# Optimization experiments

Hardware: AMD Instinct MI355X
Metric: run time of the kernel (lower is better)

The kernel has to match this reference:

```python
import jax, jax.numpy as jnp
import numpy as np

N_HEADS = 16
MAX_REL = 64  # max_relative_pos_len


def setup_inputs() -> dict:
    key = jax.random.key(0)
    ks = jax.random.split(key, 8)
    B, S, D = 2, 2048, 1024
    d = D // N_HEADS
    sc = 0.02
    return {
        "hidden_states": jax.random.normal(ks[0], (B, S, D), jnp.float32),
        "attention_mask": jnp.zeros((B, 1, 1, S), jnp.float32),
        "Wq": jax.random.normal(ks[1], (D, D), jnp.float32) * sc,
        "bq": jnp.zeros((D,), jnp.float32),
        "Wk": jax.random.normal(ks[2], (D, D), jnp.float32) * sc,
        "bk": jnp.zeros((D,), jnp.float32),
        "Wv": jax.random.normal(ks[3], (D, D), jnp.float32) * sc,
        "bv": jnp.zeros((D,), jnp.float32),
        "emb_k": jax.random.normal(ks[4], (2 * MAX_REL + 1, d), jnp.float32) * sc,
        "emb_v": jax.random.normal(ks[5], (2 * MAX_REL + 1, d), jnp.float32) * sc,
    }


def reference(hidden_states, attention_mask, Wq, bq, Wk, bk, Wv, bv, emb_k, emb_v):
    B, S, D = hidden_states.shape
    H = N_HEADS
    d = D // H
    scale = 1.0 / jnp.sqrt(jnp.asarray(d, hidden_states.dtype))

    def heads(x):  # [B,S,D] -> [B,H,S,d]
        return x.reshape(B, S, H, d).transpose(0, 2, 1, 3)

    q = heads(hidden_states @ Wq + bq)
    k = heads(hidden_states @ Wk + bk)
    v = heads(hidden_states @ Wv + bv)

    # relative position indices, clamped: [S_q, S_k]
    rel_idx = jnp.clip(jnp.arange(S)[:, None] - jnp.arange(S)[None, :], -MAX_REL, MAX_REL) + MAX_REL
    rel_k = emb_k[rel_idx]  # [S, S, d]

    # content scores + relative-key bias, both scaled by 1/sqrt(d)
    scores = (jnp.einsum('bhqd,bhkd->bhqk', q, k)
              + jnp.einsum('bhqd,qkd->bhqk', q, rel_k)) * scale
    scores = scores + attention_mask
    probs = jax.nn.softmax(scores, axis=-1)  # dropout is identity at p=0

    rel_v = emb_v[rel_idx]  # [S, S, d]
    ctx = (jnp.einsum('bhqk,bhkd->bhqd', probs, v)
           + jnp.einsum('bhqk,qkd->bhqd', probs, rel_v))
    return ctx.transpose(0, 2, 1, 3).reshape(B, S, D)
```

## Files before the change

### kernel.cpp

```cpp
#include <hip/hip_runtime.h>
#include <stdint.h>

typedef unsigned short u16;
typedef __attribute__((ext_vector_type(8))) short short8;
typedef __attribute__((ext_vector_type(4))) short s16x4;
typedef __attribute__((ext_vector_type(4))) float f32x4;
typedef __attribute__((ext_vector_type(4))) unsigned short u16x4;

#define S_LEN 2048
#define NH 16
#define DMODEL 1024
#define NR 129
#define LOG2E 1.44269504f

#define MFMA(a,b,c) __builtin_amdgcn_mfma_f32_16x16x32_bf16((a),(b),(c),0,0,0)

__device__ __forceinline__ u16 f2bf(float f){
  uint32_t u = __float_as_uint(f);
  u += 0x7fff + ((u >> 16) & 1);
  return (u16)(u >> 16);
}
__device__ __forceinline__ u16 f2bfa(float f){
  return (u16)((__float_as_uint(f) + 0x8000u) >> 16);
}
__device__ __forceinline__ float bf2f(u16 h){ return __uint_as_float(((uint32_t)h) << 16); }

__global__ __launch_bounds__(256) void k_prep(const float* __restrict__ X,
                                              const float* __restrict__ Wq, const float* __restrict__ Wk,
                                              const float* __restrict__ Wv, const float* __restrict__ Wemb,
                                              const float* __restrict__ mask,
                                              u16* __restrict__ Xb, u16* __restrict__ Wt,
                                              u16* __restrict__ Eb, float* __restrict__ maskL){
  const int bid = blockIdx.x, tid = threadIdx.x;
  if (bid < 4096){
    int i = bid * 256 + tid;
    const float4* xp = (const float4*)X;
    float4 v = xp[i];
    u16x4 o; o.x = f2bf(v.x); o.y = f2bf(v.y); o.z = f2bf(v.z); o.w = f2bf(v.w);
    *(u16x4*)(Xb + (size_t)i * 4) = o;
  } else if (bid < 4864){
    int b2 = bid - 4096;
    int z = b2 >> 8;
    const float* W = (z == 0) ? Wq : (z == 1) ? Wk : Wv;
    u16* Ot = Wt + (size_t)z * 1024 * 1024;
    __shared__ float t[64][65];
    int k0 = ((b2 >> 4) & 15) * 64, n0 = (b2 & 15) * 64;
    int c = tid & 63, r0 = (tid >> 6) * 16;
    #pragma unroll
    for (int i = 0; i < 16; ++i) t[r0 + i][c] = W[(size_t)(k0 + r0 + i) * 1024 + n0 + c];
    __syncthreads();
    #pragma unroll
    for (int i = 0; i < 16; ++i) Ot[(size_t)(n0 + r0 + i) * 1024 + k0 + c] = f2bf(t[c][r0 + i]);
  } else if (bid < 4900){
    int idx = (bid - 4864) * 256 + tid;
    if (idx < 144 * 64){
      int r = idx >> 6;
      Eb[idx] = (r < NR) ? f2bf(Wemb[idx]) : (u16)0;
    }
  } else {
    int idx = (bid - 4900) * 256 + tid;
    maskL[idx] = mask[idx] * LOG2E;
  }
}

__global__ __launch_bounds__(256) void k_qkv(const u16* __restrict__ Xb, const u16* __restrict__ Wt,
                                             const float* __restrict__ bq, const float* __restrict__ bk,
                                             const float* __restrict__ bv,
                                             u16* __restrict__ Qs, u16* __restrict__ Kb, u16* __restrict__ Vb){
  const int z = blockIdx.z;
  const u16* W = Wt + (size_t)z * 1024 * 1024;
  const float* bias = (z == 0) ? bq : (z == 1) ? bk : bv;
  u16* outp = (z == 0) ? Qs : (z == 1) ? Kb : Vb;
  const float vs = (z == 0) ? 0.125f * LOG2E : 1.0f;
  const int n0 = blockIdx.x * 128, m0 = blockIdx.y * 128;
  const int tid = threadIdx.x, w = tid >> 6, lane = tid & 63, l15 = lane & 15, quad = lane >> 4;
  const int wm = (w >> 1) * 64, wn = (w & 1) * 64;
  __shared__ __attribute__((aligned(16))) u16 As[128][40];
  __shared__ __attribute__((aligned(16))) u16 Bs[128][40];
  f32x4 acc[4][4];
  #pragma unroll
  for (int i = 0; i < 4; ++i)
    #pragma unroll
    for (int j = 0; j < 4; ++j) acc[i][j] = (f32x4){0.f,0.f,0.f,0.f};

  for (int k0 = 0; k0 < 1024; k0 += 32){
    __syncthreads();
    #pragma unroll
    for (int i = 0; i < 2; ++i){
      int c = tid + i * 256; int r = c >> 2, ch = (c & 3) * 8;
      *(short8*)&As[r][ch] = *(const short8*)(Xb + (size_t)(m0 + r) * 1024 + k0 + ch);
      *(short8*)&Bs[r][ch] = *(const short8*)(W  + (size_t)(n0 + r) * 1024 + k0 + ch);
    }
    __syncthreads();
    short8 af[4], bfr[4];
    #pragma unroll
    for (int f = 0; f < 4; ++f){
      af[f]  = *(const short8*)&As[wm + f * 16 + l15][quad * 8];
      bfr[f] = *(const short8*)&Bs[wn + f * 16 + l15][quad * 8];
    }
    #pragma unroll
    for (int i = 0; i < 4; ++i)
      #pragma unroll
      for (int j = 0; j < 4; ++j) acc[i][j] = MFMA(af[i], bfr[j], acc[i][j]);
  }
  #pragma unroll
  for (int i = 0; i < 4; ++i){
    #pragma unroll
    for (int j = 0; j < 4; ++j){
      int col = n0 + wn + j * 16 + l15;
      float bsv = bias[col];
      int hh = col >> 6, jd = col & 63;
      #pragma unroll
      for (int r = 0; r < 4; ++r){
        int row = m0 + wm + i * 16 + quad * 4 + r;
        int bb = row >> 11, s = row & 2047;
        float vv = (acc[i][j][r] + bsv) * vs;
        outp[(((size_t)(bb * 16 + hh)) * S_LEN + s) * 64 + jd] = f2bf(vv);
      }
    }
  }
}

__global__ __launch_bounds__(256) void k_transv(const u16* __restrict__ Vb, u16* __restrict__ Vt){
  const int g = blockIdx.y; const int s0 = blockIdx.x * 64;
  __shared__ __attribute__((aligned(16))) u16 t[64][72];
  const int tid = threadIdx.x;
  #pragma unroll
  for (int i = 0; i < 2; ++i){
    int c = tid + i * 256; int r = c >> 3, ch = (c & 7) * 8;
    *(short8*)&t[r][ch] = *(const short8*)(Vb + ((size_t)g * S_LEN + s0 + r) * 64 + ch);
  }
  __syncthreads();
  #pragma unroll
  for (int i = 0; i < 2; ++i){
    int c = tid + i * 256; int d = c >> 3, ch = (c & 7) * 8;
    short8 vv;
    #pragma unroll
    for (int u = 0; u < 8; ++u) vv[u] = (short)t[ch + u][d];
    *(short8*)(Vt + ((size_t)g * 64 + d) * S_LEN + s0 + ch) = vv;
  }
}

__global__ __launch_bounds__(256, 3) void k_flash(const u16* __restrict__ QS, const u16* __restrict__ KB,
                                                  const u16* __restrict__ VT, const u16* __restrict__ EMBK,
                                                  const float* __restrict__ maskL, const float* __restrict__ embv,
                                                  float* __restrict__ out){
  const int g = blockIdx.y; const int b = g >> 4; const int h = g & 15;
  const int q0 = blockIdx.x * 64;
  const int tid = threadIdx.x;
  const int w = tid >> 6; const int lane = tid & 63;
  const int l15 = lane & 15; const int quad = lane >> 4;
  const int wm = w * 16;
  const int rqb = quad * 4;
  const int qrow = q0 + wm + l15;

  __shared__ union UKE {
    struct {
      __attribute__((aligned(16))) u16 Ks[64][72];
      __attribute__((aligned(16))) u16 Vs[64][72];
    } s;
    __attribute__((aligned(16))) u16 Evs[64][136];
  } uu;
  __shared__ __attribute__((aligned(16))) u16 QEb[4][16][132];
  __shared__ __attribute__((aligned(16))) u16 Psb[64][136];

  {
    short8 z8 = (short8){0,0,0,0,0,0,0,0};
    for (int i = tid; i < 64 * 136 / 8; i += 256) ((short8*)Psb)[i] = z8;
  }

  const u16* qptr = QS + ((size_t)g * S_LEN + q0 + wm + l15) * 64 + quad * 8;
  short8 qa0 = *(const short8*)qptr;
  short8 qa1 = *(const short8*)(qptr + 32);

  #pragma unroll
  for (int fn = 0; fn < 9; ++fn){
    const u16* ep = EMBK + (fn * 16 + l15) * 64 + quad * 8;
    short8 eb0 = *(const short8*)ep;
    short8 eb1 = *(const short8*)(ep + 32);
    f32x4 c = (f32x4){0.f,0.f,0.f,0.f};
    c = MFMA(qa0, eb0, c);
    c = MFMA(qa1, eb1, c);
    int col = fn * 16 + l15;
    if (col < NR){
      #pragma unroll
      for (int r = 0; r < 4; ++r) QEb[w][rqb + r][col] = f2bf(c[r]);
    }
  }
  __syncthreads();

  const float qeR = bf2f(QEb[w][l15][0]);
  const float qeL = bf2f(QEb[w][l15][128]);

  f32x4 o[4];
  #pragma unroll
  for (int f = 0; f < 4; ++f) o[f] = (f32x4){0.f,0.f,0.f,0.f};
  float l_sum = 0.f;
  float ll0   = 0.f;
  float ll_mx = 0.f;
  float rsb_s = 0.f;

  for (int kt = 0; kt < S_LEN; kt += 64){
    __syncthreads();
    #pragma unroll
    for (int i = 0; i < 2; ++i){
      int c = tid + i * 256; int row = c >> 3, ch = (c & 7) * 8;
      *(short8*)&uu.s.Ks[row][ch] = *(const short8*)(KB + ((size_t)g * S_LEN + kt + row) * 64 + ch);
      short8 vsrc = *(const short8*)(VT + ((size_t)g * 64 + row) * S_LEN + kt + ch);
      int c0 = ((ch & 8) ? 32 : 0) + (ch >> 4) * 4;
      s16x4 lo = __builtin_shufflevector(vsrc, vsrc, 0, 1, 2, 3);
      s16x4 hi = __builtin_shufflevector(vsrc, vsrc, 4, 5, 6, 7);
      *(s16x4*)&uu.s.Vs[row][c0]      = lo;
      *(s16x4*)&uu.s.Vs[row][c0 + 16] = hi;
    }
    __syncthreads();

    f32x4 sc[4];
    #pragma unroll
    for (int fn = 0; fn < 4; ++fn){
      short8 kb0 = *(const short8*)&uu.s.Ks[fn * 16 + l15][quad * 8];
      short8 kb1 = *(const short8*)&uu.s.Ks[fn * 16 + l15][32 + quad * 8];
      f32x4 c = (f32x4){0.f,0.f,0.f,0.f};
      c = MFMA(kb0, qa0, c);
      c = MFMA(kb1, qa1, c);
      sc[fn] = c;
    }

    if (kt <= q0 - 128){
      #pragma unroll
      for (int fn = 0; fn < 4; ++fn){
        f32x4 mv = *(const f32x4*)&maskL[b * S_LEN + kt + fn * 16 + rqb];
        mv += qeL;
        #pragma unroll
        for (int r = 0; r < 4; ++r){
          float p = exp2f(sc[fn][r] + mv[r]);
          l_sum += p;
          sc[fn][r] = p;
        }
      }
    } else if (kt >= q0 + 128){
      #pragma unroll
      for (int fn = 0; fn < 4; ++fn){
        f32x4 mv = *(const f32x4*)&maskL[b * S_LEN + kt + fn * 16 + rqb];
        mv += qeR;
        #pragma unroll
        for (int r = 0; r < 4; ++r){
          float p = exp2f(sc[fn][r] + mv[r]);
          l_sum += p;
          sc[fn][r] = p;
        }
      }
    } else {
      #pragma unroll
      for (int fn = 0; fn < 4; ++fn){
        f32x4 mv = *(const f32x4*)&maskL[b * S_LEN + kt + fn * 16 + rqb];
        int kbase = kt + fn * 16 + rqb;
        #pragma unroll
        for (int r = 0; r < 4; ++r){
          int dq = qrow - (kbase + r) + 64;
          int ridx = min(max(dq, 0), 128);
          float p = exp2f(sc[fn][r] + bf2f(QEb[w][l15][ridx]) + mv[r]);
          l_sum += p;
          ll_mx += (dq >= 128) ? p : 0.f;
          if (dq >= 1 && dq <= 127){
            Psb[wm + l15][127 - dq] = f2bfa(p);
            rsb_s += p;
          }
          sc[fn][r] = p;
        }
      }
    }

    #pragma unroll
    for (int fp = 0; fp < 2; ++fp){
      short8 pa;
      #pragma unroll
      for (int r = 0; r < 4; ++r){
        pa[r]     = (short)f2bfa(sc[2 * fp][r]);
        pa[4 + r] = (short)f2bfa(sc[2 * fp + 1][r]);
      }
      #pragma unroll
      for (int fd = 0; fd < 4; ++fd){
        short8 vb = *(const short8*)&uu.s.Vs[fd * 16 + l15][quad * 16 + fp * 8];
        o[fd] = MFMA(pa, vb, o[fd]);
      }
    }

    if (kt == q0 - 128) ll0 = l_sum;
  }

  __syncthreads();
  {
    int d = tid & 63, t4 = tid >> 6;
    #pragma unroll
    for (int it = 0; it < 34; ++it){
      int t = t4 + it * 4;
      float v = (t <= 126) ? embv[(size_t)(127 - t) * 64 + d] : 0.f;
      uu.Evs[d][t] = f2bf(v);
    }
  }
  __syncthreads();

  f32x4 ob[4];
  #pragma unroll
  for (int f = 0; f < 4; ++f) ob[f] = (f32x4){0.f,0.f,0.f,0.f};
  #pragma unroll
  for (int kb = 0; kb < 4; ++kb){
    short8 pa = *(const short8*)&Psb[wm + l15][kb * 32 + quad * 8];
    #pragma unroll
    for (int fd = 0; fd < 4; ++fd){
      short8 vb = *(const short8*)&uu.Evs[fd * 16 + l15][kb * 32 + quad * 8];
      ob[fd] = MFMA(pa, vb, ob[fd]);
    }
  }

  float llv = ll0 + ll_mx;
  #pragma unroll
  for (int st = 16; st < 64; st <<= 1){
    l_sum += __shfl_xor(l_sum, st, 64);
    llv   += __shfl_xor(llv,   st, 64);
    rsb_s += __shfl_xor(rsb_s, st, 64);
  }

  float inv[4], tl[4], trr[4];
  #pragma unroll
  for (int r = 0; r < 4; ++r){
    int src = (quad << 4) + rqb + r;
    float L  = __shfl(l_sum, src, 64);
    float lv = __shfl(llv,   src, 64);
    float rv = __shfl(rsb_s, src, 64);
    inv[r] = 1.f / L;
    tl[r]  = lv * inv[r];
    trr[r] = 1.f - tl[r] - rv * inv[r];
  }

  #pragma unroll
  for (int fd = 0; fd < 4; ++fd){
    int dim = fd * 16 + l15;
    float evL = embv[(size_t)128 * 64 + dim];
    float evR = embv[dim];
    #pragma unroll
    for (int r = 0; r < 4; ++r){
      int row = q0 + wm + rqb + r;
      float val = (o[fd][r] + ob[fd][r]) * inv[r] + tl[r] * evL + trr[r] * evR;
      out[((size_t)(b * S_LEN + row)) * DMODEL + h * 64 + dim] = val;
    }
  }
}

extern "C" void kernel_launch(void* const* d_in, const int* in_sizes, int n_in,
                              void* d_out, int out_size, void* d_ws, size_t ws_size,
                              hipStream_t stream){
  const float* X    = (const float*)d_in[0];
  const float* mask = (const float*)d_in[1];
  const float* Wq   = (const float*)d_in[2];
  const float* bq   = (const float*)d_in[3];
  const float* Wk   = (const float*)d_in[4];
  const float* bk   = (const float*)d_in[5];
  const float* Wv   = (const float*)d_in[6];
  const float* bv   = (const float*)d_in[7];
  const float* embk = (const float*)d_in[8];
  const float* embv = (const float*)d_in[9];
  float* out = (float*)d_out;
  char* ws = (char*)d_ws;

  u16* XB   = (u16*)(ws + 0);
  u16* WT   = (u16*)(ws + 8388608);
  u16* EKB  = (u16*)(ws + 14680064);
  u16* QS   = (u16*)(ws + 14698496);
  u16* KB   = (u16*)(ws + 23087104);
  u16* VB   = (u16*)(ws + 31475712);
  u16* VT   = (u16*)(ws + 39864320);
  float* MSL = (float*)(ws + 48252928);

  k_prep   <<<4916, 256, 0, stream>>>(X, Wq, Wk, Wv, embk, mask, XB, WT, EKB, MSL);
  k_qkv    <<<dim3(8, 32, 3), 256, 0, stream>>>(XB, WT, bq, bk, bv, QS, KB, VB);
  k_transv <<<dim3(32, 32), 256, 0, stream>>>(VB, VT);
  k_flash  <<<dim3(32, 32), 256, 0, stream>>>(QS, KB, VT, EKB, MSL, embv, out);
}
```

Measured before the change: 263.9 us.

## Prefetch K/V tiles into registers, fold mask into MFMA, compute row sums via MFMA

The QKV GEMM now stages tiles with global_load_lds direct-to-LDS copies in an unpadded layout. The attention loop register-prefetches the next K/V tile and mask values while the current tile is processed. It seeds the QK MFMA accumulator with mask plus the relative bias and uses the hardware exp2. Row sums of P come from an extra MFMA against a ones vector instead of scalar adds, and bf16 packing uses v_cvt_pk_bf16_f32, with s_setprio around the MFMA sections. This adds register pressure, and the unpadded LDS layout may cause bank conflicts. Row sums are now taken from bf16-rounded probabilities.

Measured after the change: 213.8 us. -19.0%, faster.

```diff
diff --git a/kernel.cpp b/kernel.cpp
--- a/kernel.cpp
+++ b/kernel.cpp
@@ -24,6 +24,17 @@
   return (u16)((__float_as_uint(f) + 0x8000u) >> 16);
 }
 __device__ __forceinline__ float bf2f(u16 h){ return __uint_as_float(((uint32_t)h) << 16); }
+
+__device__ __forceinline__ uint32_t cvtpk(float lo, float hi){
+  uint32_t r;
+  asm("v_cvt_pk_bf16_f32 %0, %1, %2" : "=v"(r) : "v"(lo), "v"(hi));
+  return r;
+}
+
+__device__ __forceinline__ void gl_lds16(const u16* g, u16* l){
+  __builtin_amdgcn_global_load_lds((const __attribute__((address_space(1))) void*)g,
+                                   (__attribute__((address_space(3))) void*)l, 16, 0, 0);
+}
 
 __global__ __launch_bounds__(256) void k_prep(const float* __restrict__ X,
                                               const float* __restrict__ Wq, const float* __restrict__ Wk,
@@ -75,28 +86,32 @@
   const int n0 = blockIdx.x * 128, m0 = blockIdx.y * 128;
   const int tid = threadIdx.x, w = tid >> 6, lane = tid & 63, l15 = lane & 15, quad = lane >> 4;
   const int wm = (w >> 1) * 64, wn = (w & 1) * 64;
-  __shared__ __attribute__((aligned(16))) u16 As[128][40];
-  __shared__ __attribute__((aligned(16))) u16 Bs[128][40];
+  __shared__ __attribute__((aligned(16))) u16 As[128 * 32];
+  __shared__ __attribute__((aligned(16))) u16 Bs[128 * 32];
   f32x4 acc[4][4];
   #pragma unroll
   for (int i = 0; i < 4; ++i)
     #pragma unroll
     for (int j = 0; j < 4; ++j) acc[i][j] = (f32x4){0.f,0.f,0.f,0.f};
+
+  const int rA = lane >> 2, cA = (lane & 3) * 8;
+  const u16* aBase = Xb + (size_t)(m0 + w * 16 + rA) * 1024 + cA;
+  const u16* bBase = W  + (size_t)(n0 + w * 16 + rA) * 1024 + cA;
+  u16* aDst0 = As + (w * 16) * 32;  u16* aDst1 = As + (64 + w * 16) * 32;
+  u16* bDst0 = Bs + (w * 16) * 32;  u16* bDst1 = Bs + (64 + w * 16) * 32;
 
   for (int k0 = 0; k0 < 1024; k0 += 32){
     __syncthreads();
-    #pragma unroll
-    for (int i = 0; i < 2; ++i){
-      int c = tid + i * 256; int r = c >> 2, ch = (c & 3) * 8;
-      *(short8*)&As[r][ch] = *(const short8*)(Xb + (size_t)(m0 + r) * 1024 + k0 + ch);
-      *(short8*)&Bs[r][ch] = *(const short8*)(W  + (size_t)(n0 + r) * 1024 + k0 + ch);
-    }
+    gl_lds16(aBase + k0,             aDst0);
+    gl_lds16(aBase + 64 * 1024 + k0, aDst1);
+    gl_lds16(bBase + k0,             bDst0);
+    gl_lds16(bBase + 64 * 1024 + k0, bDst1);
     __syncthreads();
     short8 af[4], bfr[4];
     #pragma unroll
     for (int f = 0; f < 4; ++f){
-      af[f]  = *(const short8*)&As[wm + f * 16 + l15][quad * 8];
-      bfr[f] = *(const short8*)&Bs[wn + f * 16 + l15][quad * 8];
+      af[f]  = *(const short8*)(As + (wm + f * 16 + l15) * 32 + quad * 8);
+      bfr[f] = *(const short8*)(Bs + (wn + f * 16 + l15) * 32 + quad * 8);
     }
     #pragma unroll
     for (int i = 0; i < 4; ++i)
@@ -169,6 +184,22 @@
     for (int i = tid; i < 64 * 136 / 8; i += 256) ((short8*)Psb)[i] = z8;
   }
 
+  const int srow0 = tid >> 3;
+  const int srow1 = srow0 + 32;
+  const int sch = (tid & 7) * 8;
+  const int c0 = ((sch & 8) ? 32 : 0) + (sch >> 4) * 4;
+  const u16* kSrc = KB + (size_t)g * S_LEN * 64 + sch;
+  const u16* vSrc = VT + (size_t)g * 64 * S_LEN + sch;
+  const float* mBase = maskL + b * S_LEN;
+
+  short8 kr0 = *(const short8*)(kSrc + (size_t)srow0 * 64);
+  short8 kr1 = *(const short8*)(kSrc + (size_t)srow1 * 64);
+  short8 vr0 = *(const short8*)(vSrc + (size_t)srow0 * S_LEN);
+  short8 vr1 = *(const short8*)(vSrc + (size_t)srow1 * S_LEN);
+  f32x4 mcur[4];
+  #pragma unroll
+  for (int fn = 0; fn < 4; ++fn) mcur[fn] = *(const f32x4*)(mBase + fn * 16 + rqb);
+
   const u16* qptr = QS + ((size_t)g * S_LEN + q0 + wm + l15) * 64 + quad * 8;
   short8 qa0 = *(const short8*)qptr;
   short8 qa1 = *(const short8*)(qptr + 32);
@@ -192,101 +223,117 @@
   const float qeR = bf2f(QEb[w][l15][0]);
   const float qeL = bf2f(QEb[w][l15][128]);
 
+  short8 bones;
+  {
+    short one = (l15 == 0) ? (short)0x3F80 : (short)0;
+    #pragma unroll
+    for (int j = 0; j < 8; ++j) bones[j] = one;
+  }
+
   f32x4 o[4];
   #pragma unroll
   for (int f = 0; f < 4; ++f) o[f] = (f32x4){0.f,0.f,0.f,0.f};
-  float l_sum = 0.f;
-  float ll0   = 0.f;
+  f32x4 lacc = (f32x4){0.f,0.f,0.f,0.f};
+  float ll0v[4] = {0.f,0.f,0.f,0.f};
   float ll_mx = 0.f;
   float rsb_s = 0.f;
 
   for (int kt = 0; kt < S_LEN; kt += 64){
     __syncthreads();
-    #pragma unroll
-    for (int i = 0; i < 2; ++i){
-      int c = tid + i * 256; int row = c >> 3, ch = (c & 7) * 8;
-      *(short8*)&uu.s.Ks[row][ch] = *(const short8*)(KB + ((size_t)g * S_LEN + kt + row) * 64 + ch);
-      short8 vsrc = *(const short8*)(VT + ((size_t)g * 64 + row) * S_LEN + kt + ch);
-      int c0 = ((ch & 8) ? 32 : 0) + (ch >> 4) * 4;
-      s16x4 lo = __builtin_shufflevector(vsrc, vsrc, 0, 1, 2, 3);
-      s16x4 hi = __builtin_shufflevector(vsrc, vsrc, 4, 5, 6, 7);
-      *(s16x4*)&uu.s.Vs[row][c0]      = lo;
-      *(s16x4*)&uu.s.Vs[row][c0 + 16] = hi;
+    *(short8*)&uu.s.Ks[srow0][sch] = kr0;
+    *(short8*)&uu.s.Ks[srow1][sch] = kr1;
+    {
+      s16x4 lo = __builtin_shufflevector(vr0, vr0, 0, 1, 2, 3);
+      s16x4 hi = __builtin_shufflevector(vr0, vr0, 4, 5, 6, 7);
+      *(s16x4*)&uu.s.Vs[srow0][c0]      = lo;
+      *(s16x4*)&uu.s.Vs[srow0][c0 + 16] = hi;
+    }
+    {
+      s16x4 lo = __builtin_shufflevector(vr1, vr1, 0, 1, 2, 3);
+      s16x4 hi = __builtin_shufflevector(vr1, vr1, 4, 5, 6, 7);
+      *(s16x4*)&uu.s.Vs[srow1][c0]      = lo;
+      *(s16x4*)&uu.s.Vs[srow1][c0 + 16] = hi;
     }
     __syncthreads();
 
-    f32x4 sc[4];
+    const int ktn = kt + 64;
+    f32x4 mnext[4];
+    if (ktn < S_LEN){
+      kr0 = *(const short8*)(kSrc + (size_t)(ktn + srow0) * 64);
+      kr1 = *(const short8*)(kSrc + (size_t)(ktn + srow1) * 64);
+      vr0 = *(const short8*)(vSrc + (size_t)srow0 * S_LEN + ktn);
+      vr1 = *(const short8*)(vSrc + (size_t)srow1 * S_LEN + ktn);
+      #pragma unroll
+      for (int fn = 0; fn < 4; ++fn) mnext[fn] = *(const f32x4*)(mBase + ktn + fn * 16 + rqb);
+    }
+
+    const bool leftC  = (kt <= q0 - 128);
+    const bool rightC = (kt >= q0 + 128);
+    const float qeadd = leftC ? qeL : (rightC ? qeR : 0.f);
+
+    f32x4 p4[4];
+    __builtin_amdgcn_s_setprio(1);
     #pragma unroll
     for (int fn = 0; fn < 4; ++fn){
       short8 kb0 = *(const short8*)&uu.s.Ks[fn * 16 + l15][quad * 8];
       short8 kb1 = *(const short8*)&uu.s.Ks[fn * 16 + l15][32 + quad * 8];
-      f32x4 c = (f32x4){0.f,0.f,0.f,0.f};
+      f32x4 c = mcur[fn] + qeadd;
       c = MFMA(kb0, qa0, c);
       c = MFMA(kb1, qa1, c);
-      sc[fn] = c;
-    }
-
-    if (kt <= q0 - 128){
+      p4[fn] = c;
+    }
+    __builtin_amdgcn_s_setprio(0);
+
+    if (leftC | rightC){
+      #pragma unroll
+      for (int fn = 0; fn < 4; ++fn)
+        #pragma unroll
+        for (int r = 0; r < 4; ++r) p4[fn][r] = __builtin_amdgcn_exp2f(p4[fn][r]);
+    } else {
       #pragma unroll
       for (int fn = 0; fn < 4; ++fn){
-        f32x4 mv = *(const f32x4*)&maskL[b * S_LEN + kt + fn * 16 + rqb];
-        mv += qeL;
-        #pragma unroll
-        for (int r = 0; r < 4; ++r){
-          float p = exp2f(sc[fn][r] + mv[r]);
-          l_sum += p;
-          sc[fn][r] = p;
-        }
-      }
-    } else if (kt >= q0 + 128){
-      #pragma unroll
-      for (int fn = 0; fn < 4; ++fn){
-        f32x4 mv = *(const f32x4*)&maskL[b * S_LEN + kt + fn * 16 + rqb];
-        mv += qeR;
-        #pragma unroll
-        for (int r = 0; r < 4; ++r){
-          float p = exp2f(sc[fn][r] + mv[r]);
-          l_sum += p;
-          sc[fn][r] = p;
-        }
-      }
-    } else {
-      #pragma unroll
-      for (int fn = 0; fn < 4; ++fn){
-        f32x4 mv = *(const f32x4*)&maskL[b * S_LEN + kt + fn * 16 + rqb];
         int kbase = kt + fn * 16 + rqb;
         #pragma unroll
         for (int r = 0; r < 4; ++r){
           int dq = qrow - (kbase + r) + 64;
           int ridx = min(max(dq, 0), 128);
-          float p = exp2f(sc[fn][r] + bf2f(QEb[w][l15][ridx]) + mv[r]);
-          l_sum += p;
+          float p = __builtin_amdgcn_exp2f(p4[fn][r] + bf2f(QEb[w][l15][ridx]));
           ll_mx += (dq >= 128) ? p : 0.f;
           if (dq >= 1 && dq <= 127){
             Psb[wm + l15][127 - dq] = f2bfa(p);
             rsb_s += p;
           }
-          sc[fn][r] = p;
+          p4[fn][r] = p;
         }
       }
     }
 
+    __builtin_amdgcn_s_setprio(1);
     #pragma unroll
     for (int fp = 0; fp < 2; ++fp){
-      short8 pa;
-      #pragma unroll
-      for (int r = 0; r < 4; ++r){
-        pa[r]     = (short)f2bfa(sc[2 * fp][r]);
-        pa[4 + r] = (short)f2bfa(sc[2 * fp + 1][r]);
-      }
+      union { uint32_t u[4]; short8 s8; } pk;
+      pk.u[0] = cvtpk(p4[2 * fp][0],     p4[2 * fp][1]);
+      pk.u[1] = cvtpk(p4[2 * fp][2],     p4[2 * fp][3]);
+      pk.u[2] = cvtpk(p4[2 * fp + 1][0], p4[2 * fp + 1][1]);
+      pk.u[3] = cvtpk(p4[2 * fp + 1][2], p4[2 * fp + 1][3]);
+      short8 pa = pk.s8;
+      lacc = MFMA(pa, bones, lacc);
       #pragma unroll
       for (int fd = 0; fd < 4; ++fd){
         short8 vb = *(const short8*)&uu.s.Vs[fd * 16 + l15][quad * 16 + fp * 8];
         o[fd] = MFMA(pa, vb, o[fd]);
       }
     }
-
-    if (kt == q0 - 128) ll0 = l_sum;
+    __builtin_amdgcn_s_setprio(0);
+
+    if (kt == q0 - 128){
+      #pragma unroll
+      for (int r = 0; r < 4; ++r) ll0v[r] = lacc[r];
+    }
+    if (ktn < S_LEN){
+      #pragma unroll
+      for (int fn = 0; fn < 4; ++fn) mcur[fn] = mnext[fn];
+    }
   }
 
   __syncthreads();
@@ -314,23 +361,22 @@
     }
   }
 
-  float llv = ll0 + ll_mx;
   #pragma unroll
   for (int st = 16; st < 64; st <<= 1){
-    l_sum += __shfl_xor(l_sum, st, 64);
-    llv   += __shfl_xor(llv,   st, 64);
+    ll_mx += __shfl_xor(ll_mx, st, 64);
     rsb_s += __shfl_xor(rsb_s, st, 64);
   }
 
   float inv[4], tl[4], trr[4];
   #pragma unroll
   for (int r = 0; r < 4; ++r){
-    int src = (quad << 4) + rqb + r;
-    float L  = __shfl(l_sum, src, 64);
-    float lv = __shfl(llv,   src, 64);
-    float rv = __shfl(rsb_s, src, 64);
+    float L   = __shfl(lacc[r], quad << 4);
+    float l0  = __shfl(ll0v[r], quad << 4);
+    int src   = (quad << 4) + rqb + r;
+    float lmx = __shfl(ll_mx, src);
+    float rv  = __shfl(rsb_s, src);
     inv[r] = 1.f / L;
-    tl[r]  = lv * inv[r];
+    tl[r]  = (l0 + lmx) * inv[r];
     trr[r] = 1.f - tl[r] - rv * inv[r];
   }
 
```
